# Performance work log

Measured on AMD Instinct MI355X. Metric: run time of the kernel, lower is better.

The kernel has to match this reference:

```python
import jax, jax.numpy as jnp
import numpy as np
from jax import lax

C = 256
HEADS = 8
H2 = HEADS // 2          # heads per branch
HD = C // HEADS          # head dim = 32
SR = 4                   # spatial reduction ratio
WS = 7                   # window size (hard-coded in source)
SCALE = HD ** -0.5
EPS = 1e-5


def _window_partition(t, H, W, D):
    # t: [B, h, N, c] -> [B*h*nW, WS^3, c]
    B, h, N, c = t.shape
    t = t.reshape(B * h, H // WS, WS, W // WS, WS, D // WS, WS, c)
    t = t.transpose(0, 1, 3, 5, 2, 4, 6, 7)
    return t.reshape(-1, WS * WS * WS, c)


def _window_reverse(w, H, W, D, head):
    # w: [BH*nW, WS^3, c] -> [B, N, head*c] (heads interleaved into channels)
    nW = (H // WS) * (W // WS) * (D // WS)
    BH = w.shape[0] // nW
    x = w.reshape(BH, H // WS, W // WS, D // WS, WS, WS, WS, -1)
    x = x.transpose(0, 1, 4, 2, 5, 3, 6, 7).reshape(BH, H, W, D, -1)
    B = BH // head
    x = x.reshape(B, head, H, W, D, -1).transpose(0, 2, 3, 4, 1, 5)
    return x.reshape(B, H * W * D, -1)


def setup_inputs() -> dict:
    key = jax.random.key(0)
    ks = jax.random.split(key, 16)
    B, H, W, D = 1, 28, 28, 28
    N = H * W * D
    tn = lambda k, shp: jax.random.normal(k, shp, jnp.float32) * 0.02
    # conv fan-out inits (per source _init_weights)
    lepe_fan = 3 * 3 * C // C  # depthwise: groups=C
    sr_fan = SR * SR * C
    return {
        "x": jax.random.normal(ks[0], (B, N, C), jnp.float32),
        "H": H, "W": W, "D": D,
        "lepe_w": tn(ks[1], (C, C)),
        "lepe_b": jnp.zeros((C,), jnp.float32),
        "lepe_conv_w": jax.random.normal(ks[2], (C, 1, 3, 3, 3), jnp.float32) * np.sqrt(2.0 / lepe_fan),
        "lepe_conv_b": jnp.zeros((C,), jnp.float32),
        "sr_w": jax.random.normal(ks[3], (C, C, SR, SR, SR), jnp.float32) * np.sqrt(2.0 / sr_fan),
        "sr_b": jnp.zeros((C,), jnp.float32),
        "norm_g": jnp.ones((C,), jnp.float32),
        "norm_b": jnp.zeros((C,), jnp.float32),
        "q1_w": tn(ks[4], (C // 2, C)),
        "kv1_w": tn(ks[5], (C, C)),
        "q2_w": tn(ks[6], (C // 2, C)),
        "kv2_w": tn(ks[7], (C, C)),
        "proj_w": tn(ks[8], (C, C)),
        "proj_b": jnp.zeros((C,), jnp.float32),
    }


def _forward(x, lepe_w, lepe_b, lepe_conv_w, lepe_conv_b, sr_w, sr_b,
             norm_g, norm_b, q1_w, kv1_w, q2_w, kv2_w, proj_w, proj_b,
             H, W, D):
    B, N, _ = x.shape
    # --- LePE: linear -> depthwise Conv3d over (H,W,D) ---
    y = x @ lepe_w.T + lepe_b                              # [B,N,C]
    y = y.transpose(0, 2, 1).reshape(B, C, H, W, D)
    lepe = lax.conv_general_dilated(
        y, lepe_conv_w, window_strides=(1, 1, 1), padding='SAME',
        dimension_numbers=('NCDHW', 'OIDHW', 'NCDHW'), feature_group_count=C)
    lepe = (lepe + lepe_conv_b[None, :, None, None, None])
    lepe = lepe.reshape(B, C, N).transpose(0, 2, 1)        # [B,N,C]

    x_ = x.transpose(0, 2, 1).reshape(B, C, H, W, D)

    # --- Branch 1: spatially-reduced global attention (heads 0..3) ---
    q1 = (x @ q1_w.T).reshape(B, N, H2, HD).transpose(0, 2, 1, 3)   # [B,h2,N,hd]
    x1 = lax.conv_general_dilated(
        x_, sr_w, window_strides=(SR, SR, SR), padding='VALID',
        dimension_numbers=('NCDHW', 'OIDHW', 'NCDHW'))
    x1 = x1 + sr_b[None, :, None, None, None]
    x1 = x1.reshape(B, C, -1).transpose(0, 2, 1)                    # [B,Nr,C]
    mu = x1.mean(-1, keepdims=True)
    var = ((x1 - mu) ** 2).mean(-1, keepdims=True)
    x1 = (x1 - mu) * lax.rsqrt(var + EPS) * norm_g + norm_b
    x1 = jax.nn.gelu(x1, approximate=False)
    Nr = x1.shape[1]
    kv1 = (x1 @ kv1_w.T).reshape(B, Nr, 2, H2, HD).transpose(2, 0, 3, 1, 4)
    k1, v1 = kv1[0], kv1[1]                                         # [B,h2,Nr,hd]
    attn1 = jax.nn.softmax(jnp.einsum('bhnd,bhmd->bhnm', q1, k1) * SCALE, axis=-1)
    o1 = jnp.einsum('bhnm,bhmd->bhnd', attn1, v1)
    o1 = o1.transpose(0, 2, 1, 3).reshape(B, N, C // 2)

    # --- Branch 2: windowed local attention (heads 4..7) ---
    q2 = (x @ q2_w.T).reshape(B, N, H2, HD).transpose(0, 2, 1, 3)
    kv2 = (x @ kv2_w.T).reshape(B, N, 2, H2, HD).transpose(2, 0, 3, 1, 4)
    k2, v2 = kv2[0], kv2[1]                                         # [B,h2,N,hd]
    q2w = _window_partition(q2, H, W, D)
    k2w = _window_partition(k2, H, W, D)
    v2w = _window_partition(v2, H, W, D)
    attn2 = jax.nn.softmax(jnp.einsum('wnd,wmd->wnm', q2w, k2w) * SCALE, axis=-1)
    o2 = jnp.einsum('wnm,wmd->wnd', attn2, v2w)
    o2 = _window_reverse(o2, H, W, D, H2)                           # [B,N,C/2]

    out = jnp.concatenate([o1, o2], axis=-1)
    return (out + lepe) @ proj_w.T + proj_b


def reference(x, H, W, D, lepe_w, lepe_b, lepe_conv_w, lepe_conv_b,
              sr_w, sr_b, norm_g, norm_b, q1_w, kv1_w, q2_w, kv2_w,
              proj_w, proj_b):
    return _forward(x, lepe_w, lepe_b, lepe_conv_w, lepe_conv_b, sr_w, sr_b,
                    norm_g, norm_b, q1_w, kv1_w, q2_w, kv2_w, proj_w, proj_b,
                    int(H), int(W), int(D))
```

## Files before the change

kernel.cpp:

```cpp
#include <hip/hip_runtime.h>

#define N_TOK 21952
#define NR    343
#define ATT_SCALE 0.17677669529663687f

typedef unsigned short u16;
typedef short  v8s __attribute__((ext_vector_type(8)));
typedef float  v4f __attribute__((ext_vector_type(4)));

__device__ __forceinline__ float bf2f(unsigned u) {
    return __builtin_bit_cast(float, u << 16);
}
__device__ __forceinline__ u16 f2bf(float f) {
    unsigned u = __builtin_bit_cast(unsigned, f);
    u += 0x7fffu + ((u >> 16) & 1u);
    return (u16)(u >> 16);
}
__device__ __forceinline__ unsigned bfadd2(unsigned a, unsigned b) {
    float lo = bf2f(a & 0xffffu) + bf2f(b & 0xffffu);
    float hi = bf2f(a >> 16)     + bf2f(b >> 16);
    return (unsigned)f2bf(lo) | ((unsigned)f2bf(hi) << 16);
}

__global__ __launch_bounds__(256) void convert_x_kernel(
    const float* __restrict__ x, u16* __restrict__ xb)
{
    size_t i = ((size_t)blockIdx.x * 256 + threadIdx.x) * 8;
    float4 a0 = *(const float4*)(x + i);
    float4 a1 = *(const float4*)(x + i + 4);
    uint4 av;
    av.x = (unsigned)f2bf(a0.x) | ((unsigned)f2bf(a0.y) << 16);
    av.y = (unsigned)f2bf(a0.z) | ((unsigned)f2bf(a0.w) << 16);
    av.z = (unsigned)f2bf(a1.x) | ((unsigned)f2bf(a1.y) << 16);
    av.w = (unsigned)f2bf(a1.z) | ((unsigned)f2bf(a1.w) << 16);
    *(uint4*)(xb + i) = av;
}

#define WSEG0 16384
#define WSEG1 24576
#define WSEG2 32768
#define WSEG3 49152
#define WSEG4 65536
#define WSEG5 81920
#define WSEG6 82112

__global__ __launch_bounds__(256) void convert_w_kernel(
    const float* __restrict__ wl,  const float* __restrict__ wq1,
    const float* __restrict__ wq2, const float* __restrict__ wk2,
    const float* __restrict__ wk1, const float* __restrict__ wp,
    const float* __restrict__ lepe_b,
    u16* wb_comb, u16* wb_k1, u16* wb_p, float* bias_all)
{
    int gid = blockIdx.x * 256 + threadIdx.x;
    if (gid >= WSEG6) return;
    if (gid >= WSEG5) {
        int b = gid - WSEG5;
        float4 v;
        int i = b * 4;
        v.x = (i + 0 < 256) ? lepe_b[i + 0] : 0.f;
        v.y = (i + 1 < 256) ? lepe_b[i + 1] : 0.f;
        v.z = (i + 2 < 256) ? lepe_b[i + 2] : 0.f;
        v.w = (i + 3 < 256) ? lepe_b[i + 3] : 0.f;
        *(float4*)(bias_all + i) = v;
        return;
    }
    const float* s; u16* d; int l; float sc = 1.f;
    if      (gid < WSEG0) { s = wl;  d = wb_comb;           l = gid; }
    else if (gid < WSEG1) { s = wq1; d = wb_comb + 65536;   l = gid - WSEG0; sc = ATT_SCALE; }
    else if (gid < WSEG2) { s = wq2; d = wb_comb + 98304;   l = gid - WSEG1; sc = ATT_SCALE; }
    else if (gid < WSEG3) { s = wk2; d = wb_comb + 131072;  l = gid - WSEG2; }
    else if (gid < WSEG4) { s = wk1; d = wb_k1;             l = gid - WSEG3; }
    else                  { s = wp;  d = wb_p;              l = gid - WSEG4; }
    float4 v = *(const float4*)(s + (size_t)l * 4);
    *(ushort4*)(d + (size_t)l * 4) =
        make_ushort4(f2bf(v.x * sc), f2bf(v.y * sc), f2bf(v.z * sc), f2bf(v.w * sc));
}

__global__ __launch_bounds__(256) void convert_sr_kernel(
    const float* __restrict__ wsr, u16* __restrict__ wt)
{
    int u  = blockIdx.x * 256 + threadIdx.x;
    int co = u >> 8, ci = u & 255;
    const float* src = wsr + (size_t)co * 16384 + ci * 64;
#pragma unroll
    for (int t4 = 0; t4 < 16; t4++) {
        float4 v = *(const float4*)(src + t4 * 4);
        int t = t4 * 4;
        wt[(size_t)(t + 0) * 65536 + co * 256 + ci] = f2bf(v.x);
        wt[(size_t)(t + 1) * 65536 + co * 256 + ci] = f2bf(v.y);
        wt[(size_t)(t + 2) * 65536 + co * 256 + ci] = f2bf(v.z);
        wt[(size_t)(t + 3) * 65536 + co * 256 + ci] = f2bf(v.w);
    }
}

#define LDA 40

__global__ __launch_bounds__(256, 4) void gemm_pipe(
    const u16* __restrict__ A, const u16* __restrict__ A2,
    const u16* __restrict__ W, const float* __restrict__ bias,
    void* __restrict__ outp, int M, int ldout, int mode, int nwg, int NT)
{
    __shared__ u16 Asm[2][128 * LDA];
    __shared__ u16 Bsm[2][64 * LDA];
    const int tid = threadIdx.x;

    int bid = blockIdx.x;
    int q = nwg >> 3, r8 = nwg & 7;
    int xcd = bid & 7, idx = bid >> 3;
    int wgid = (xcd < r8 ? xcd * (q + 1) : r8 * (q + 1) + (xcd - r8) * q) + idx;
    const int m0 = (wgid / NT) * 128;
    const int n0 = (wgid % NT) * 64;

    const int wave = tid >> 6, lane = tid & 63;
    const int wm = (wave & 1) * 64, wn = (wave >> 1) * 32;
    const int fr = lane & 15, fq = lane >> 4;

    const int ar0 = tid >> 2;
    const int ar1 = ar0 + 64;
    const int seg = (tid & 3) * 8;
    const bool g0 = (m0 + ar0) < M;
    const bool g1 = (m0 + ar1) < M;
    const u16* pA0 = A + (size_t)(m0 + ar0) * 256 + seg;
    const u16* pA1 = A + (size_t)(m0 + ar1) * 256 + seg;
    const u16* pB  = W + (size_t)(n0 + ar0) * 256 + seg;
    const u16* pC0 = A2 + (size_t)(m0 + ar0) * 256 + seg;
    const u16* pC1 = A2 + (size_t)(m0 + ar1) * 256 + seg;

    uint4 ra0, ra1, rb, rc0, rc1;
    const bool has2 = (A2 != nullptr);

    auto LOAD = [&](int ph) {
        int kk = ph * 32;
        ra0 = g0 ? *(const uint4*)(pA0 + kk) : make_uint4(0, 0, 0, 0);
        ra1 = g1 ? *(const uint4*)(pA1 + kk) : make_uint4(0, 0, 0, 0);
        rb  = *(const uint4*)(pB + kk);
        if (has2) {
            rc0 = g0 ? *(const uint4*)(pC0 + kk) : make_uint4(0, 0, 0, 0);
            rc1 = g1 ? *(const uint4*)(pC1 + kk) : make_uint4(0, 0, 0, 0);
        }
    };
    auto WRITE = [&](int buf) {
        uint4 a0 = ra0, a1 = ra1;
        if (has2) {
            a0.x = bfadd2(a0.x, rc0.x); a0.y = bfadd2(a0.y, rc0.y);
            a0.z = bfadd2(a0.z, rc0.z); a0.w = bfadd2(a0.w, rc0.w);
            a1.x = bfadd2(a1.x, rc1.x); a1.y = bfadd2(a1.y, rc1.y);
            a1.z = bfadd2(a1.z, rc1.z); a1.w = bfadd2(a1.w, rc1.w);
        }
        *(uint4*)(Asm[buf] + ar0 * LDA + seg) = a0;
        *(uint4*)(Asm[buf] + ar1 * LDA + seg) = a1;
        *(uint4*)(Bsm[buf] + ar0 * LDA + seg) = rb;
    };

    v4f acc[4][2];
#pragma unroll
    for (int i = 0; i < 4; i++)
#pragma unroll
        for (int j = 0; j < 2; j++) acc[i][j] = (v4f){0.f, 0.f, 0.f, 0.f};

    LOAD(0);
    WRITE(0);
    __syncthreads();

    int cur = 0;
    for (int ph = 0; ph < 8; ph++) {
        if (ph + 1 < 8) LOAD(ph + 1);
        {
            v8s af[4], bf[2];
#pragma unroll
            for (int i = 0; i < 4; i++)
                af[i] = *(const v8s*)(Asm[cur] + (wm + i * 16 + fr) * LDA + fq * 8);
#pragma unroll
            for (int j = 0; j < 2; j++)
                bf[j] = *(const v8s*)(Bsm[cur] + (wn + j * 16 + fr) * LDA + fq * 8);
#pragma unroll
            for (int i = 0; i < 4; i++)
#pragma unroll
                for (int j = 0; j < 2; j++)
                    acc[i][j] = __builtin_amdgcn_mfma_f32_16x16x32_bf16(
                        af[i], bf[j], acc[i][j], 0, 0, 0);
        }
        if (ph + 1 < 8) WRITE(cur ^ 1);
        __syncthreads();
        cur ^= 1;
    }

    float* outf = (float*)outp;
    u16*   outb = (u16*)outp;
#pragma unroll
    for (int i = 0; i < 4; i++) {
#pragma unroll
        for (int j = 0; j < 2; j++) {
            int col = n0 + wn + j * 16 + fr;
#pragma unroll
            for (int rr = 0; rr < 4; rr++) {
                int row = m0 + wm + i * 16 + fq * 4 + rr;
                if (row >= M) continue;
                float v = acc[i][j][rr];
                if (bias) v += bias[col];
                if (mode == 0) outb[(size_t)row * ldout + col] = f2bf(v);
                else           outf[(size_t)row * ldout + col] = v;
            }
        }
    }
}

__global__ __launch_bounds__(256) void sr_gemm(
    const u16* __restrict__ xb, const u16* __restrict__ Wt,
    float* __restrict__ partials)
{
    __shared__ u16 Asm[128 * LDA];
    __shared__ u16 Bsm[64 * LDA];
    const int tid = threadIdx.x;
    const int m0 = blockIdx.x * 128;
    const int n0 = blockIdx.y * 64;
    const int z  = blockIdx.z;
    const int wave = tid >> 6, lane = tid & 63;
    const int wm = (wave & 1) * 64, wn = (wave >> 1) * 32;
    const int fr = lane & 15, fq = lane >> 4;

    v4f acc[4][2];
#pragma unroll
    for (int i = 0; i < 4; i++)
#pragma unroll
        for (int j = 0; j < 2; j++) acc[i][j] = (v4f){0.f, 0.f, 0.f, 0.f};

    for (int it = 0; it < 16; it++) {
        int tap = z * 2 + (it >> 3);
        int ci0 = (it & 7) * 32;
        int kz = tap >> 4, ky = (tap >> 2) & 3, kx = tap & 3;
#pragma unroll
        for (int i = 0; i < 2; i++) {
            int u = tid + i * 256;
            int r = u >> 2, seg = (u & 3) * 8;
            uint4 av = make_uint4(0, 0, 0, 0);
            int p = m0 + r;
            if (p < NR) {
                int pz = p / 49, pr = p % 49, py = pr / 7, px = pr % 7;
                int n = (pz * 4 + kz) * 784 + (py * 4 + ky) * 28 + (px * 4 + kx);
                av = *(const uint4*)(xb + (size_t)n * 256 + ci0 + seg);
            }
            *(uint4*)(Asm + r * LDA + seg) = av;
        }
        {
            int r = tid >> 2, seg = (tid & 3) * 8;
            uint4 wv = *(const uint4*)(Wt + (size_t)tap * 65536 +
                                       (size_t)(n0 + r) * 256 + ci0 + seg);
            *(uint4*)(Bsm + r * LDA + seg) = wv;
        }
        __syncthreads();

        v8s af[4], bfr[2];
#pragma unroll
        for (int i = 0; i < 4; i++)
            af[i] = *(const v8s*)(Asm + (wm + i * 16 + fr) * LDA + fq * 8);
#pragma unroll
        for (int j = 0; j < 2; j++)
            bfr[j] = *(const v8s*)(Bsm + (wn + j * 16 + fr) * LDA + fq * 8);
#pragma unroll
        for (int i = 0; i < 4; i++)
#pragma unroll
            for (int j = 0; j < 2; j++)
                acc[i][j] = __builtin_amdgcn_mfma_f32_16x16x32_bf16(
                    af[i], bfr[j], acc[i][j], 0, 0, 0);
        __syncthreads();
    }

    float* dst = partials + (size_t)z * (NR * 256);
#pragma unroll
    for (int i = 0; i < 4; i++) {
#pragma unroll
        for (int j = 0; j < 2; j++) {
            int col = n0 + wn + j * 16 + fr;
#pragma unroll
            for (int r = 0; r < 4; r++) {
                int row = m0 + wm + i * 16 + fq * 4 + r;
                if (row < NR) dst[(size_t)row * 256 + col] = acc[i][j][r];
            }
        }
    }
}

__global__ __launch_bounds__(256) void ln_gelu_kernel(
    const float* __restrict__ partials, const float* __restrict__ srb,
    const float* __restrict__ g, const float* __restrict__ b,
    u16* __restrict__ out)
{
    int row = blockIdx.x, c = threadIdx.x;
    float v = srb[c];
#pragma unroll
    for (int s = 0; s < 32; s++)
        v += partials[(size_t)s * (NR * 256) + row * 256 + c];
    float s1 = v, s2 = v * v;
#pragma unroll
    for (int off = 1; off < 64; off <<= 1) {
        s1 += __shfl_xor(s1, off);
        s2 += __shfl_xor(s2, off);
    }
    __shared__ float ws[4], ws2[4];
    int wave = c >> 6, lane = c & 63;
    if (lane == 0) { ws[wave] = s1; ws2[wave] = s2; }
    __syncthreads();
    float mean = (ws[0] + ws[1] + ws[2] + ws[3]) * (1.f / 256.f);
    float m2   = (ws2[0] + ws2[1] + ws2[2] + ws2[3]) * (1.f / 256.f);
    float var  = m2 - mean * mean;
    float xn = (v - mean) * rsqrtf(var + 1e-5f) * g[c] + b[c];
    out[row * 256 + c] = f2bf(0.5f * xn * (1.f + erff(xn * 0.70710678118654752f)));
}

__global__ __launch_bounds__(256) void dwconv_kernel(
    const u16* __restrict__ xall, const float* __restrict__ w,
    const float* __restrict__ bias, u16* __restrict__ out)
{
    __shared__ float sm[216 * 64];
    __shared__ float sw[64 * 27];
    const int tid = threadIdx.x;
    const int t  = blockIdx.x;
    const int g  = blockIdx.y;
    const int tz = t / 49, tr = t % 49, ty = tr / 7, tx = tr % 7;

    for (int u = tid; u < 64 * 27; u += 256) sw[u] = w[g * 64 * 27 + u];

    for (int u = tid; u < 216 * 8; u += 256) {
        int r = u >> 3, c8 = (u & 7) * 8;
        int vz = tz * 4 - 1 + r / 36;
        int rem = r % 36;
        int vy = ty * 4 - 1 + rem / 6;
        int vx = tx * 4 - 1 + rem % 6;
        float f[8];
        if ((unsigned)vz < 28u && (unsigned)vy < 28u && (unsigned)vx < 28u) {
            int n = vz * 784 + vy * 28 + vx;
            uint4 raw = *(const uint4*)(xall + (size_t)n * 768 + g * 64 + c8);
            f[0] = bf2f(raw.x & 0xffffu); f[1] = bf2f(raw.x >> 16);
            f[2] = bf2f(raw.y & 0xffffu); f[3] = bf2f(raw.y >> 16);
            f[4] = bf2f(raw.z & 0xffffu); f[5] = bf2f(raw.z >> 16);
            f[6] = bf2f(raw.w & 0xffffu); f[7] = bf2f(raw.w >> 16);
        } else {
#pragma unroll
            for (int i = 0; i < 8; i++) f[i] = 0.f;
        }
        float* dst = &sm[r * 64 + c8];
        *(float4*)dst       = make_float4(f[0], f[1], f[2], f[3]);
        *(float4*)(dst + 4) = make_float4(f[4], f[5], f[6], f[7]);
    }
    __syncthreads();

    const int c  = tid & 63;
    const int ch = g * 64 + c;
    float wreg[27];
#pragma unroll
    for (int j = 0; j < 27; j++) wreg[j] = sw[c * 27 + j];
    const float bc = bias[ch];

    const int vbase = (tid >> 6) * 16;
    for (int v = vbase; v < vbase + 16; v++) {
        int vz = v >> 4, vy = (v >> 2) & 3, vx = v & 3;
        float a = bc;
#pragma unroll
        for (int dz = 0; dz < 3; dz++)
#pragma unroll
            for (int dy = 0; dy < 3; dy++)
#pragma unroll
                for (int dx = 0; dx < 3; dx++)
                    a = fmaf(sm[((vz + dz) * 36 + (vy + dy) * 6 + (vx + dx)) * 64 + c],
                             wreg[dz * 9 + dy * 3 + dx], a);
        int n = (tz * 4 + vz) * 784 + (ty * 4 + vy) * 28 + (tx * 4 + vx);
        out[(size_t)n * 256 + ch] = f2bf(a);
    }
}

#define KP  40
#define VTP 360
#define PP  40

__global__ __launch_bounds__(256) void attn1_kernel(
    const u16* __restrict__ xall, const u16* __restrict__ kv1,
    u16* __restrict__ o)
{
    __shared__ u16 Ks[352 * KP];
    __shared__ u16 VTs[32 * VTP];
    __shared__ u16 Ps[4 * 16 * PP];
    const int tid = threadIdx.x;
    const int h = blockIdx.y;
    const int qbase = blockIdx.x * 352;
    const int mt0 = blockIdx.z * 11;
    const int wave = tid >> 6, lane = tid & 63;
    const int fr = lane & 15, fq = lane >> 4;

    for (int u = tid; u < 352 * 4; u += 256) {
        int r = u >> 2, seg = u & 3;
        uint4 kq = make_uint4(0, 0, 0, 0), vq = make_uint4(0, 0, 0, 0);
        if (r < NR) {
            kq = *(const uint4*)(kv1 + (size_t)r * 256 + h * 32 + seg * 8);
            vq = *(const uint4*)(kv1 + (size_t)r * 256 + 128 + h * 32 + seg * 8);
        }
        *(uint4*)(Ks + r * KP + seg * 8) = kq;
        int d0 = seg * 8;
        VTs[(d0 + 0) * VTP + r] = (u16)(vq.x & 0xffffu);
        VTs[(d0 + 1) * VTP + r] = (u16)(vq.x >> 16);
        VTs[(d0 + 2) * VTP + r] = (u16)(vq.y & 0xffffu);
        VTs[(d0 + 3) * VTP + r] = (u16)(vq.y >> 16);
        VTs[(d0 + 4) * VTP + r] = (u16)(vq.z & 0xffffu);
        VTs[(d0 + 5) * VTP + r] = (u16)(vq.z >> 16);
        VTs[(d0 + 6) * VTP + r] = (u16)(vq.w & 0xffffu);
        VTs[(d0 + 7) * VTP + r] = (u16)(vq.w >> 16);
    }
    __syncthreads();

    u16* Pw = Ps + wave * 16 * PP;
    for (int mt = mt0 + wave; mt < mt0 + 11; mt += 4) {
        int qrow = qbase + mt * 16 + fr;
        v8s aq = {0, 0, 0, 0, 0, 0, 0, 0};
        if (qrow < N_TOK)
            aq = *(const v8s*)(xall + (size_t)qrow * 768 + 256 + h * 32 + fq * 8);

        v4f s[22];
#pragma unroll
        for (int t = 0; t < 22; t++) {
            v8s bk = *(const v8s*)(Ks + (t * 16 + fr) * KP + fq * 8);
            s[t] = __builtin_amdgcn_mfma_f32_16x16x32_bf16(
                aq, bk, (v4f){0.f, 0.f, 0.f, 0.f}, 0, 0, 0);
        }
        if (fr >= 7) {
#pragma unroll
            for (int r = 0; r < 4; r++) s[21][r] = -1e30f;
        }

        float inv_l[4];
#pragma unroll
        for (int r = 0; r < 4; r++) {
            float m = s[0][r];
#pragma unroll
            for (int t = 1; t < 22; t++) m = fmaxf(m, s[t][r]);
#pragma unroll
            for (int off = 1; off < 16; off <<= 1) m = fmaxf(m, __shfl_xor(m, off));
            float l = 0.f;
#pragma unroll
            for (int t = 0; t < 22; t++) {
                v4f sv = s[t];
                float p = __expf(sv[r] - m);
                sv[r] = p; s[t] = sv;
                l += p;
            }
#pragma unroll
            for (int off = 1; off < 16; off <<= 1) l += __shfl_xor(l, off);
            inv_l[r] = 1.f / l;
        }

        v4f o0 = {0.f, 0.f, 0.f, 0.f}, o1 = {0.f, 0.f, 0.f, 0.f};
#pragma unroll
        for (int kt = 0; kt < 11; kt++) {
#pragma unroll
            for (int tt = 0; tt < 2; tt++) {
                int t = kt * 2 + tt;
#pragma unroll
                for (int r = 0; r < 4; r++)
                    Pw[(fq * 4 + r) * PP + tt * 16 + fr] = f2bf(s[t][r]);
            }
            __asm__ volatile("s_waitcnt lgkmcnt(0)" ::: "memory");
            v8s ap  = *(const v8s*)(Pw + fr * PP + fq * 8);
            v8s bv0 = *(const v8s*)(VTs + fr * VTP + kt * 32 + fq * 8);
            v8s bv1 = *(const v8s*)(VTs + (16 + fr) * VTP + kt * 32 + fq * 8);
            o0 = __builtin_amdgcn_mfma_f32_16x16x32_bf16(ap, bv0, o0, 0, 0, 0);
            o1 = __builtin_amdgcn_mfma_f32_16x16x32_bf16(ap, bv1, o1, 0, 0, 0);
        }

#pragma unroll
        for (int r = 0; r < 4; r++) {
            int n = qbase + mt * 16 + fq * 4 + r;
            if (n < N_TOK) {
                u16* op = o + (size_t)n * 256 + h * 32;
                op[fr]      = f2bf(o0[r] * inv_l[r]);
                op[16 + fr] = f2bf(o1[r] * inv_l[r]);
            }
        }
    }
}

__global__ __launch_bounds__(256) void attn2_kernel(
    const u16* __restrict__ xall, u16* __restrict__ o)
{
    __shared__ u16 Ks[352 * KP];
    __shared__ u16 VTs[32 * VTP];
    __shared__ u16 Ps[4 * 16 * PP];
    const int tid = threadIdx.x;
    const int h  = blockIdx.y;
    const int wi = blockIdx.x;
    const int zb = (wi >> 4) & 3, yb = (wi >> 2) & 3, xb = wi & 3;
    const int mt0 = blockIdx.z * 11;
    const int wave = tid >> 6, lane = tid & 63;
    const int fr = lane & 15, fq = lane >> 4;

    for (int u = tid; u < 352 * 4; u += 256) {
        int r = u >> 2, seg = u & 3;
        uint4 kq = make_uint4(0, 0, 0, 0), vq = make_uint4(0, 0, 0, 0);
        if (r < NR) {
            int mz = r / 49, mr = r % 49, my = mr / 7, mx = mr % 7;
            int nk = (zb * 7 + mz) * 784 + (yb * 7 + my) * 28 + (xb * 7 + mx);
            const u16* base = xall + (size_t)nk * 768 + 512;
            kq = *(const uint4*)(base + h * 32 + seg * 8);
            vq = *(const uint4*)(base + 128 + h * 32 + seg * 8);
        }
        *(uint4*)(Ks + r * KP + seg * 8) = kq;
        int d0 = seg * 8;
        VTs[(d0 + 0) * VTP + r] = (u16)(vq.x & 0xffffu);
        VTs[(d0 + 1) * VTP + r] = (u16)(vq.x >> 16);
        VTs[(d0 + 2) * VTP + r] = (u16)(vq.y & 0xffffu);
        VTs[(d0 + 3) * VTP + r] = (u16)(vq.y >> 16);
        VTs[(d0 + 4) * VTP + r] = (u16)(vq.z & 0xffffu);
        VTs[(d0 + 5) * VTP + r] = (u16)(vq.z >> 16);
        VTs[(d0 + 6) * VTP + r] = (u16)(vq.w & 0xffffu);
        VTs[(d0 + 7) * VTP + r] = (u16)(vq.w >> 16);
    }
    __syncthreads();

    u16* Pw = Ps + wave * 16 * PP;
    for (int mt = mt0 + wave; mt < mt0 + 11; mt += 4) {
        int tw = mt * 16 + fr;
        v8s aq = {0, 0, 0, 0, 0, 0, 0, 0};
        if (tw < NR) {
            int wz = tw / 49, tr2 = tw % 49, wy = tr2 / 7, wx = tr2 % 7;
            int nq = (zb * 7 + wz) * 784 + (yb * 7 + wy) * 28 + (xb * 7 + wx);
            aq = *(const v8s*)(xall + (size_t)nq * 768 + 384 + h * 32 + fq * 8);
        }

        v4f s[22];
#pragma unroll
        for (int t = 0; t < 22; t++) {
            v8s bk = *(const v8s*)(Ks + (t * 16 + fr) * KP + fq * 8);
            s[t] = __builtin_amdgcn_mfma_f32_16x16x32_bf16(
                aq, bk, (v4f){0.f, 0.f, 0.f, 0.f}, 0, 0, 0);
        }
        if (fr >= 7) {
#pragma unroll
            for (int r = 0; r < 4; r++) s[21][r] = -1e30f;
        }

        float inv_l[4];
#pragma unroll
        for (int r = 0; r < 4; r++) {
            float m = s[0][r];
#pragma unroll
            for (int t = 1; t < 22; t++) m = fmaxf(m, s[t][r]);
#pragma unroll
            for (int off = 1; off < 16; off <<= 1) m = fmaxf(m, __shfl_xor(m, off));
            float l = 0.f;
#pragma unroll
            for (int t = 0; t < 22; t++) {
                v4f sv = s[t];
                float p = __expf(sv[r] - m);
                sv[r] = p; s[t] = sv;
                l += p;
            }
#pragma unroll
            for (int off = 1; off < 16; off <<= 1) l += __shfl_xor(l, off);
            inv_l[r] = 1.f / l;
        }

        v4f o0 = {0.f, 0.f, 0.f, 0.f}, o1 = {0.f, 0.f, 0.f, 0.f};
#pragma unroll
        for (int kt = 0; kt < 11; kt++) {
#pragma unroll
            for (int tt = 0; tt < 2; tt++) {
                int t = kt * 2 + tt;
#pragma unroll
                for (int r = 0; r < 4; r++)
                    Pw[(fq * 4 + r) * PP + tt * 16 + fr] = f2bf(s[t][r]);
            }
            __asm__ volatile("s_waitcnt lgkmcnt(0)" ::: "memory");
            v8s ap  = *(const v8s*)(Pw + fr * PP + fq * 8);
            v8s bv0 = *(const v8s*)(VTs + fr * VTP + kt * 32 + fq * 8);
            v8s bv1 = *(const v8s*)(VTs + (16 + fr) * VTP + kt * 32 + fq * 8);
            o0 = __builtin_amdgcn_mfma_f32_16x16x32_bf16(ap, bv0, o0, 0, 0, 0);
            o1 = __builtin_amdgcn_mfma_f32_16x16x32_bf16(ap, bv1, o1, 0, 0, 0);
        }

#pragma unroll
        for (int r = 0; r < 4; r++) {
            int ts = mt * 16 + fq * 4 + r;
            if (ts < NR) {
                int wz = ts / 49, tr2 = ts % 49, wy = tr2 / 7, wx = tr2 % 7;
                int nq = (zb * 7 + wz) * 784 + (yb * 7 + wy) * 28 + (xb * 7 + wx);
                u16* op = o + (size_t)nq * 256 + 128 + h * 32;
                op[fr]      = f2bf(o0[r] * inv_l[r]);
                op[16 + fr] = f2bf(o1[r] * inv_l[r]);
            }
        }
    }
}

extern "C" void kernel_launch(void* const* d_in, const int* in_sizes, int n_in,
                              void* d_out, int out_size, void* d_ws, size_t ws_size,
                              hipStream_t stream)
{
    const float* x       = (const float*)d_in[0];
    const float* lepe_w  = (const float*)d_in[4];
    const float* lepe_b  = (const float*)d_in[5];
    const float* lconv_w = (const float*)d_in[6];
    const float* lconv_b = (const float*)d_in[7];
    const float* sr_w    = (const float*)d_in[8];
    const float* sr_b    = (const float*)d_in[9];
    const float* norm_g  = (const float*)d_in[10];
    const float* norm_b  = (const float*)d_in[11];
    const float* q1_w    = (const float*)d_in[12];
    const float* kv1_w   = (const float*)d_in[13];
    const float* q2_w    = (const float*)d_in[14];
    const float* kv2_w   = (const float*)d_in[15];
    const float* proj_w  = (const float*)d_in[16];
    const float* proj_b  = (const float*)d_in[17];
    float* out = (float*)d_out;

    const size_t NC = (size_t)N_TOK * 256;

    float* partials = (float*)d_ws;
    float* bias_all = partials + 32 * (NR * 256);
    u16* xb     = (u16*)(bias_all + 768);
    u16* xall   = xb + NC;
    u16* lepeb  = xall + (size_t)N_TOK * 768;
    u16* colb   = lepeb + NC;
    u16* x1b    = colb + NC;
    u16* kv1b   = x1b + NR * 256;
    u16* wb_comb = kv1b + NR * 256;
    u16* wb_k1  = wb_comb + 196608;
    u16* wb_p   = wb_k1 + 65536;
    u16* wsr_t  = wb_p + 65536;
    size_t need = (size_t)(32 * NR * 256 + 768) * 4 +
                  (NC + (size_t)N_TOK * 768 + 3 * NC + 2 * (size_t)NR * 256 +
                   196608 + 2 * 65536 + 4194304) * 2;
    if (ws_size < need) return;

    convert_w_kernel<<<dim3(321), 256, 0, stream>>>(
        lepe_w, q1_w, q2_w, kv2_w, kv1_w, proj_w, lepe_b,
        wb_comb, wb_k1, wb_p, bias_all);
    convert_sr_kernel<<<dim3(256), 256, 0, stream>>>(sr_w, wsr_t);
    convert_x_kernel<<<dim3(2744), 256, 0, stream>>>(x, xb);
    gemm_pipe<<<dim3(172 * 12), 256, 0, stream>>>(
        xb, nullptr, wb_comb, bias_all, xall, N_TOK, 768, 0, 172 * 12, 12);
    dwconv_kernel<<<dim3(343, 4), 256, 0, stream>>>(xall, lconv_w, lconv_b, lepeb);
    sr_gemm<<<dim3(3, 4, 32), 256, 0, stream>>>(xb, wsr_t, partials);
    ln_gelu_kernel<<<dim3(NR), 256, 0, stream>>>(partials, sr_b, norm_g, norm_b, x1b);
    gemm_pipe<<<dim3(3 * 4), 256, 0, stream>>>(
        x1b, nullptr, wb_k1, nullptr, kv1b, NR, 256, 0, 3 * 4, 4);
    attn1_kernel<<<dim3(63, 4, 2), 256, 0, stream>>>(xall, kv1b, colb);
    attn2_kernel<<<dim3(64, 4, 2), 256, 0, stream>>>(xall, colb);
    gemm_pipe<<<dim3(172 * 4), 256, 0, stream>>>(
        colb, lepeb, wb_p, proj_b, out, N_TOK, 256, 1, 172 * 4, 4);
}
```

Before: 272.7 us.

## Deepen GEMM prefetch, double-buffer SR GEMM, merge attention kernels into one launch

```diff
diff --git a/kernel.cpp b/kernel.cpp
--- a/kernel.cpp
+++ b/kernel.cpp
@@ -95,7 +95,8 @@
 
 #define LDA 40
 
-__global__ __launch_bounds__(256, 4) void gemm_pipe(
+template<bool HAS2>
+__global__ __launch_bounds__(256, 3) void gemm_pipe(
     const u16* __restrict__ A, const u16* __restrict__ A2,
     const u16* __restrict__ W, const float* __restrict__ bias,
     void* __restrict__ outp, int M, int ldout, int mode, int nwg, int NT)
@@ -123,34 +124,31 @@
     const u16* pA0 = A + (size_t)(m0 + ar0) * 256 + seg;
     const u16* pA1 = A + (size_t)(m0 + ar1) * 256 + seg;
     const u16* pB  = W + (size_t)(n0 + ar0) * 256 + seg;
-    const u16* pC0 = A2 + (size_t)(m0 + ar0) * 256 + seg;
-    const u16* pC1 = A2 + (size_t)(m0 + ar1) * 256 + seg;
-
-    uint4 ra0, ra1, rb, rc0, rc1;
-    const bool has2 = (A2 != nullptr);
-
-    auto LOAD = [&](int ph) {
-        int kk = ph * 32;
-        ra0 = g0 ? *(const uint4*)(pA0 + kk) : make_uint4(0, 0, 0, 0);
-        ra1 = g1 ? *(const uint4*)(pA1 + kk) : make_uint4(0, 0, 0, 0);
-        rb  = *(const uint4*)(pB + kk);
-        if (has2) {
-            rc0 = g0 ? *(const uint4*)(pC0 + kk) : make_uint4(0, 0, 0, 0);
-            rc1 = g1 ? *(const uint4*)(pC1 + kk) : make_uint4(0, 0, 0, 0);
-        }
-    };
-    auto WRITE = [&](int buf) {
-        uint4 a0 = ra0, a1 = ra1;
-        if (has2) {
-            a0.x = bfadd2(a0.x, rc0.x); a0.y = bfadd2(a0.y, rc0.y);
-            a0.z = bfadd2(a0.z, rc0.z); a0.w = bfadd2(a0.w, rc0.w);
-            a1.x = bfadd2(a1.x, rc1.x); a1.y = bfadd2(a1.y, rc1.y);
-            a1.z = bfadd2(a1.z, rc1.z); a1.w = bfadd2(a1.w, rc1.w);
-        }
-        *(uint4*)(Asm[buf] + ar0 * LDA + seg) = a0;
-        *(uint4*)(Asm[buf] + ar1 * LDA + seg) = a1;
-        *(uint4*)(Bsm[buf] + ar0 * LDA + seg) = rb;
-    };
+    const u16* pC0 = HAS2 ? A2 + (size_t)(m0 + ar0) * 256 + seg : nullptr;
+    const u16* pC1 = HAS2 ? A2 + (size_t)(m0 + ar1) * 256 + seg : nullptr;
+
+    uint4 rA0[2], rA1[2], rB[2], rC0[2], rC1[2];
+    const uint4 Z = make_uint4(0, 0, 0, 0);
+
+#define G_LOAD(s, ph) do { int kk = (ph) * 32;                               \
+        rA0[s] = g0 ? *(const uint4*)(pA0 + kk) : Z;                         \
+        rA1[s] = g1 ? *(const uint4*)(pA1 + kk) : Z;                         \
+        rB[s]  = *(const uint4*)(pB + kk);                                   \
+        if (HAS2) {                                                          \
+            rC0[s] = g0 ? *(const uint4*)(pC0 + kk) : Z;                     \
+            rC1[s] = g1 ? *(const uint4*)(pC1 + kk) : Z;                     \
+        } } while (0)
+
+#define L_WRITE(s, buf) do { uint4 a0 = rA0[s], a1 = rA1[s];                 \
+        if (HAS2) {                                                          \
+            a0.x = bfadd2(a0.x, rC0[s].x); a0.y = bfadd2(a0.y, rC0[s].y);    \
+            a0.z = bfadd2(a0.z, rC0[s].z); a0.w = bfadd2(a0.w, rC0[s].w);    \
+            a1.x = bfadd2(a1.x, rC1[s].x); a1.y = bfadd2(a1.y, rC1[s].y);    \
+            a1.z = bfadd2(a1.z, rC1[s].z); a1.w = bfadd2(a1.w, rC1[s].w);    \
+        }                                                                    \
+        *(uint4*)(Asm[buf] + ar0 * LDA + seg) = a0;                          \
+        *(uint4*)(Asm[buf] + ar1 * LDA + seg) = a1;                          \
+        *(uint4*)(Bsm[buf] + ar0 * LDA + seg) = rB[s]; } while (0)
 
     v4f acc[4][2];
 #pragma unroll
@@ -158,13 +156,15 @@
 #pragma unroll
         for (int j = 0; j < 2; j++) acc[i][j] = (v4f){0.f, 0.f, 0.f, 0.f};
 
-    LOAD(0);
-    WRITE(0);
+    G_LOAD(0, 0);
+    G_LOAD(1, 1);
+    L_WRITE(0, 0);
     __syncthreads();
 
-    int cur = 0;
+#pragma unroll
     for (int ph = 0; ph < 8; ph++) {
-        if (ph + 1 < 8) LOAD(ph + 1);
+        const int cur = ph & 1;
+        if (ph + 2 < 8) G_LOAD(cur, ph + 2);
         {
             v8s af[4], bf[2];
 #pragma unroll
@@ -180,10 +180,11 @@
                     acc[i][j] = __builtin_amdgcn_mfma_f32_16x16x32_bf16(
                         af[i], bf[j], acc[i][j], 0, 0, 0);
         }
-        if (ph + 1 < 8) WRITE(cur ^ 1);
+        if (ph + 1 < 8) L_WRITE(cur ^ 1, cur ^ 1);
         __syncthreads();
-        cur ^= 1;
-    }
+    }
+#undef G_LOAD
+#undef L_WRITE
 
     float* outf = (float*)outp;
     u16*   outb = (u16*)outp;
@@ -209,8 +210,8 @@
     const u16* __restrict__ xb, const u16* __restrict__ Wt,
     float* __restrict__ partials)
 {
-    __shared__ u16 Asm[128 * LDA];
-    __shared__ u16 Bsm[64 * LDA];
+    __shared__ u16 Asm[2][128 * LDA];
+    __shared__ u16 Bsm[2][64 * LDA];
     const int tid = threadIdx.x;
     const int m0 = blockIdx.x * 128;
     const int n0 = blockIdx.y * 64;
@@ -219,51 +220,64 @@
     const int wm = (wave & 1) * 64, wn = (wave >> 1) * 32;
     const int fr = lane & 15, fq = lane >> 4;
 
-    v4f acc[4][2];
-#pragma unroll
-    for (int i = 0; i < 4; i++)
-#pragma unroll
-        for (int j = 0; j < 2; j++) acc[i][j] = (v4f){0.f, 0.f, 0.f, 0.f};
-
-    for (int it = 0; it < 16; it++) {
+    const int r0 = tid >> 2;
+    const int r1 = r0 + 64;
+    const int seg = (tid & 3) * 8;
+    const int p0 = m0 + r0, p1 = m0 + r1;
+    const int pz0 = p0 / 49, pr0 = p0 % 49, py0 = pr0 / 7, px0 = pr0 % 7;
+    const int pz1 = p1 / 49, pr1 = p1 % 49, py1 = pr1 / 7, px1 = pr1 % 7;
+    const int nb0 = pz0 * 4 * 784 + py0 * 4 * 28 + px0 * 4;
+    const int nb1 = pz1 * 4 * 784 + py1 * 4 * 28 + px1 * 4;
+
+    uint4 rv0, rv1, rbv;
+    const uint4 Z = make_uint4(0, 0, 0, 0);
+
+    auto G_LOAD = [&](int it) {
         int tap = z * 2 + (it >> 3);
         int ci0 = (it & 7) * 32;
         int kz = tap >> 4, ky = (tap >> 2) & 3, kx = tap & 3;
-#pragma unroll
-        for (int i = 0; i < 2; i++) {
-            int u = tid + i * 256;
-            int r = u >> 2, seg = (u & 3) * 8;
-            uint4 av = make_uint4(0, 0, 0, 0);
-            int p = m0 + r;
-            if (p < NR) {
-                int pz = p / 49, pr = p % 49, py = pr / 7, px = pr % 7;
-                int n = (pz * 4 + kz) * 784 + (py * 4 + ky) * 28 + (px * 4 + kx);
-                av = *(const uint4*)(xb + (size_t)n * 256 + ci0 + seg);
-            }
-            *(uint4*)(Asm + r * LDA + seg) = av;
-        }
+        int koff = kz * 784 + ky * 28 + kx;
+        rv0 = (p0 < NR) ? *(const uint4*)(xb + (size_t)(nb0 + koff) * 256 + ci0 + seg) : Z;
+        rv1 = (p1 < NR) ? *(const uint4*)(xb + (size_t)(nb1 + koff) * 256 + ci0 + seg) : Z;
+        rbv = *(const uint4*)(Wt + (size_t)tap * 65536 + (size_t)(n0 + r0) * 256 + ci0 + seg);
+    };
+    auto L_WRITE = [&](int buf) {
+        *(uint4*)(Asm[buf] + r0 * LDA + seg) = rv0;
+        *(uint4*)(Asm[buf] + r1 * LDA + seg) = rv1;
+        *(uint4*)(Bsm[buf] + r0 * LDA + seg) = rbv;
+    };
+
+    v4f acc[4][2];
+#pragma unroll
+    for (int i = 0; i < 4; i++)
+#pragma unroll
+        for (int j = 0; j < 2; j++) acc[i][j] = (v4f){0.f, 0.f, 0.f, 0.f};
+
+    G_LOAD(0);
+    L_WRITE(0);
+    __syncthreads();
+
+    int cur = 0;
+    for (int it = 0; it < 16; it++) {
+        if (it + 1 < 16) G_LOAD(it + 1);
         {
-            int r = tid >> 2, seg = (tid & 3) * 8;
-            uint4 wv = *(const uint4*)(Wt + (size_t)tap * 65536 +
-                                       (size_t)(n0 + r) * 256 + ci0 + seg);
-            *(uint4*)(Bsm + r * LDA + seg) = wv;
-        }
+            v8s af[4], bfr[2];
+#pragma unroll
+            for (int i = 0; i < 4; i++)
+                af[i] = *(const v8s*)(Asm[cur] + (wm + i * 16 + fr) * LDA + fq * 8);
+#pragma unroll
+            for (int j = 0; j < 2; j++)
+                bfr[j] = *(const v8s*)(Bsm[cur] + (wn + j * 16 + fr) * LDA + fq * 8);
+#pragma unroll
+            for (int i = 0; i < 4; i++)
+#pragma unroll
+                for (int j = 0; j < 2; j++)
+                    acc[i][j] = __builtin_amdgcn_mfma_f32_16x16x32_bf16(
+                        af[i], bfr[j], acc[i][j], 0, 0, 0);
+        }
+        if (it + 1 < 16) L_WRITE(cur ^ 1);
         __syncthreads();
-
-        v8s af[4], bfr[2];
-#pragma unroll
-        for (int i = 0; i < 4; i++)
-            af[i] = *(const v8s*)(Asm + (wm + i * 16 + fr) * LDA + fq * 8);
-#pragma unroll
-        for (int j = 0; j < 2; j++)
-            bfr[j] = *(const v8s*)(Bsm + (wn + j * 16 + fr) * LDA + fq * 8);
-#pragma unroll
-        for (int i = 0; i < 4; i++)
-#pragma unroll
-            for (int j = 0; j < 2; j++)
-                acc[i][j] = __builtin_amdgcn_mfma_f32_16x16x32_bf16(
-                    af[i], bfr[j], acc[i][j], 0, 0, 0);
-        __syncthreads();
+        cur ^= 1;
     }
 
     float* dst = partials + (size_t)z * (NR * 256);
@@ -373,7 +387,7 @@
 #define VTP 360
 #define PP  40
 
-__global__ __launch_bounds__(256) void attn1_kernel(
+__global__ __launch_bounds__(256) void attn_kernel(
     const u16* __restrict__ xall, const u16* __restrict__ kv1,
     u16* __restrict__ o)
 {
@@ -381,8 +395,12 @@
     __shared__ u16 VTs[32 * VTP];
     __shared__ u16 Ps[4 * 16 * PP];
     const int tid = threadIdx.x;
-    const int h = blockIdx.y;
-    const int qbase = blockIdx.x * 352;
+    const int h  = blockIdx.y;
+    const int bx = blockIdx.x;
+    const bool br1 = bx < 63;
+    const int qbase = bx * 352;
+    const int wi = bx - 63;
+    const int zb = (wi >> 4) & 3, yb = (wi >> 2) & 3, xw = wi & 3;
     const int mt0 = blockIdx.z * 11;
     const int wave = tid >> 6, lane = tid & 63;
     const int fr = lane & 15, fq = lane >> 4;
@@ -391,8 +409,16 @@
         int r = u >> 2, seg = u & 3;
         uint4 kq = make_uint4(0, 0, 0, 0), vq = make_uint4(0, 0, 0, 0);
         if (r < NR) {
-            kq = *(const uint4*)(kv1 + (size_t)r * 256 + h * 32 + seg * 8);
-            vq = *(const uint4*)(kv1 + (size_t)r * 256 + 128 + h * 32 + seg * 8);
+            const u16* kb;
+            if (br1) {
+                kb = kv1 + (size_t)r * 256 + h * 32;
+            } else {
+                int mz = r / 49, mr = r % 49, my = mr / 7, mx = mr % 7;
+                int nk = (zb * 7 + mz) * 784 + (yb * 7 + my) * 28 + (xw * 7 + mx);
+                kb = xall + (size_t)nk * 768 + 512 + h * 32;
+            }
+            kq = *(const uint4*)(kb + seg * 8);
+            vq = *(const uint4*)(kb + 128 + seg * 8);
         }
         *(uint4*)(Ks + r * KP + seg * 8) = kq;
         int d0 = seg * 8;
@@ -409,10 +435,19 @@
 
     u16* Pw = Ps + wave * 16 * PP;
     for (int mt = mt0 + wave; mt < mt0 + 11; mt += 4) {
-        int qrow = qbase + mt * 16 + fr;
         v8s aq = {0, 0, 0, 0, 0, 0, 0, 0};
-        if (qrow < N_TOK)
-            aq = *(const v8s*)(xall + (size_t)qrow * 768 + 256 + h * 32 + fq * 8);
+        if (br1) {
+            int qrow = qbase + mt * 16 + fr;
+            if (qrow < N_TOK)
+                aq = *(const v8s*)(xall + (size_t)qrow * 768 + 256 + h * 32 + fq * 8);
+        } else {
+            int tw = mt * 16 + fr;
+            if (tw < NR) {
+                int wz = tw / 49, tr2 = tw % 49, wy = tr2 / 7, wx = tr2 % 7;
+                int nq = (zb * 7 + wz) * 784 + (yb * 7 + wy) * 28 + (xw * 7 + wx);
+                aq = *(const v8s*)(xall + (size_t)nq * 768 + 384 + h * 32 + fq * 8);
+            }
+        }
 
         v4f s[22];
 #pragma unroll
@@ -467,121 +502,19 @@
 
 #pragma unroll
         for (int r = 0; r < 4; r++) {
-            int n = qbase + mt * 16 + fq * 4 + r;
-            if (n < N_TOK) {
-                u16* op = o + (size_t)n * 256 + h * 32;
-                op[fr]      = f2bf(o0[r] * inv_l[r]);
-                op[16 + fr] = f2bf(o1[r] * inv_l[r]);
-            }
-        }
-    }
-}
-
-__global__ __launch_bounds__(256) void attn2_kernel(
-    const u16* __restrict__ xall, u16* __restrict__ o)
-{
-    __shared__ u16 Ks[352 * KP];
-    __shared__ u16 VTs[32 * VTP];
-    __shared__ u16 Ps[4 * 16 * PP];
-    const int tid = threadIdx.x;
-    const int h  = blockIdx.y;
-    const int wi = blockIdx.x;
-    const int zb = (wi >> 4) & 3, yb = (wi >> 2) & 3, xb = wi & 3;
-    const int mt0 = blockIdx.z * 11;
-    const int wave = tid >> 6, lane = tid & 63;
-    const int fr = lane & 15, fq = lane >> 4;
-
-    for (int u = tid; u < 352 * 4; u += 256) {
-        int r = u >> 2, seg = u & 3;
-        uint4 kq = make_uint4(0, 0, 0, 0), vq = make_uint4(0, 0, 0, 0);
-        if (r < NR) {
-            int mz = r / 49, mr = r % 49, my = mr / 7, mx = mr % 7;
-            int nk = (zb * 7 + mz) * 784 + (yb * 7 + my) * 28 + (xb * 7 + mx);
-            const u16* base = xall + (size_t)nk * 768 + 512;
-            kq = *(const uint4*)(base + h * 32 + seg * 8);
-            vq = *(const uint4*)(base + 128 + h * 32 + seg * 8);
-        }
-        *(uint4*)(Ks + r * KP + seg * 8) = kq;
-        int d0 = seg * 8;
-        VTs[(d0 + 0) * VTP + r] = (u16)(vq.x & 0xffffu);
-        VTs[(d0 + 1) * VTP + r] = (u16)(vq.x >> 16);
-        VTs[(d0 + 2) * VTP + r] = (u16)(vq.y & 0xffffu);
-        VTs[(d0 + 3) * VTP + r] = (u16)(vq.y >> 16);
-        VTs[(d0 + 4) * VTP + r] = (u16)(vq.z & 0xffffu);
-        VTs[(d0 + 5) * VTP + r] = (u16)(vq.z >> 16);
-        VTs[(d0 + 6) * VTP + r] = (u16)(vq.w & 0xffffu);
-        VTs[(d0 + 7) * VTP + r] = (u16)(vq.w >> 16);
-    }
-    __syncthreads();
-
-    u16* Pw = Ps + wave * 16 * PP;
-    for (int mt = mt0 + wave; mt < mt0 + 11; mt += 4) {
-        int tw = mt * 16 + fr;
-        v8s aq = {0, 0, 0, 0, 0, 0, 0, 0};
-        if (tw < NR) {
-            int wz = tw / 49, tr2 = tw % 49, wy = tr2 / 7, wx = tr2 % 7;
-            int nq = (zb * 7 + wz) * 784 + (yb * 7 + wy) * 28 + (xb * 7 + wx);
-            aq = *(const v8s*)(xall + (size_t)nq * 768 + 384 + h * 32 + fq * 8);
-        }
-
-        v4f s[22];
-#pragma unroll
-        for (int t = 0; t < 22; t++) {
-            v8s bk = *(const v8s*)(Ks + (t * 16 + fr) * KP + fq * 8);
-            s[t] = __builtin_amdgcn_mfma_f32_16x16x32_bf16(
-                aq, bk, (v4f){0.f, 0.f, 0.f, 0.f}, 0, 0, 0);
-        }
-        if (fr >= 7) {
-#pragma unroll
-            for (int r = 0; r < 4; r++) s[21][r] = -1e30f;
-        }
-
-        float inv_l[4];
-#pragma unroll
-        for (int r = 0; r < 4; r++) {
-            float m = s[0][r];
-#pragma unroll
-            for (int t = 1; t < 22; t++) m = fmaxf(m, s[t][r]);
-#pragma unroll
-            for (int off = 1; off < 16; off <<= 1) m = fmaxf(m, __shfl_xor(m, off));
-            float l = 0.f;
-#pragma unroll
-            for (int t = 0; t < 22; t++) {
-                v4f sv = s[t];
-                float p = __expf(sv[r] - m);
-                sv[r] = p; s[t] = sv;
-                l += p;
-            }
-#pragma unroll
-            for (int off = 1; off < 16; off <<= 1) l += __shfl_xor(l, off);
-            inv_l[r] = 1.f / l;
-        }
-
-        v4f o0 = {0.f, 0.f, 0.f, 0.f}, o1 = {0.f, 0.f, 0.f, 0.f};
-#pragma unroll
-        for (int kt = 0; kt < 11; kt++) {
-#pragma unroll
-            for (int tt = 0; tt < 2; tt++) {
-                int t = kt * 2 + tt;
-#pragma unroll
-                for (int r = 0; r < 4; r++)
-                    Pw[(fq * 4 + r) * PP + tt * 16 + fr] = f2bf(s[t][r]);
-            }
-            __asm__ volatile("s_waitcnt lgkmcnt(0)" ::: "memory");
-            v8s ap  = *(const v8s*)(Pw + fr * PP + fq * 8);
-            v8s bv0 = *(const v8s*)(VTs + fr * VTP + kt * 32 + fq * 8);
-            v8s bv1 = *(const v8s*)(VTs + (16 + fr) * VTP + kt * 32 + fq * 8);
-            o0 = __builtin_amdgcn_mfma_f32_16x16x32_bf16(ap, bv0, o0, 0, 0, 0);
-            o1 = __builtin_amdgcn_mfma_f32_16x16x32_bf16(ap, bv1, o1, 0, 0, 0);
-        }
-
-#pragma unroll
-        for (int r = 0; r < 4; r++) {
-            int ts = mt * 16 + fq * 4 + r;
-            if (ts < NR) {
-                int wz = ts / 49, tr2 = ts % 49, wy = tr2 / 7, wx = tr2 % 7;
-                int nq = (zb * 7 + wz) * 784 + (yb * 7 + wy) * 28 + (xb * 7 + wx);
-                u16* op = o + (size_t)nq * 256 + 128 + h * 32;
+            int rloc = mt * 16 + fq * 4 + r;
+            u16* op = nullptr;
+            if (br1) {
+                int n = qbase + rloc;
+                if (n < N_TOK) op = o + (size_t)n * 256 + h * 32;
+            } else {
+                if (rloc < NR) {
+                    int wz = rloc / 49, tr2 = rloc % 49, wy = tr2 / 7, wx = tr2 % 7;
+                    int nq = (zb * 7 + wz) * 784 + (yb * 7 + wy) * 28 + (xw * 7 + wx);
+                    op = o + (size_t)nq * 256 + 128 + h * 32;
+                }
+            }
+            if (op) {
                 op[fr]      = f2bf(o0[r] * inv_l[r]);
                 op[16 + fr] = f2bf(o1[r] * inv_l[r]);
             }
@@ -634,15 +567,14 @@
         wb_comb, wb_k1, wb_p, bias_all);
     convert_sr_kernel<<<dim3(256), 256, 0, stream>>>(sr_w, wsr_t);
     convert_x_kernel<<<dim3(2744), 256, 0, stream>>>(x, xb);
-    gemm_pipe<<<dim3(172 * 12), 256, 0, stream>>>(
+    gemm_pipe<false><<<dim3(172 * 12), 256, 0, stream>>>(
         xb, nullptr, wb_comb, bias_all, xall, N_TOK, 768, 0, 172 * 12, 12);
     dwconv_kernel<<<dim3(343, 4), 256, 0, stream>>>(xall, lconv_w, lconv_b, lepeb);
     sr_gemm<<<dim3(3, 4, 32), 256, 0, stream>>>(xb, wsr_t, partials);
     ln_gelu_kernel<<<dim3(NR), 256, 0, stream>>>(partials, sr_b, norm_g, norm_b, x1b);
-    gemm_pipe<<<dim3(3 * 4), 256, 0, stream>>>(
+    gemm_pipe<false><<<dim3(3 * 4), 256, 0, stream>>>(
         x1b, nullptr, wb_k1, nullptr, kv1b, NR, 256, 0, 3 * 4, 4);
-    attn1_kernel<<<dim3(63, 4, 2), 256, 0, stream>>>(xall, kv1b, colb);
-    attn2_kernel<<<dim3(64, 4, 2), 256, 0, stream>>>(xall, colb);
-    gemm_pipe<<<dim3(172 * 4), 256, 0, stream>>>(
+    attn_kernel<<<dim3(127, 4, 2), 256, 0, stream>>>(xall, kv1b, colb);
+    gemm_pipe<true><<<dim3(172 * 4), 256, 0, stream>>>(
         colb, lepeb, wb_p, proj_b, out, N_TOK, 256, 1, 172 * 4, 4);
 }
```

Measured after the change: 288.6 us. 5.8% more time.
